# Kernel tuning notes

Hardware: AMD Instinct MI355X
Metric: run time of the kernel (lower is better)

The kernel has to match this reference:

```python
import jax, jax.numpy as jnp
import numpy as np

INPUT_SIZE = 512
HIDDEN = 1024
OUT = 4
SEQ = 2048


def setup_inputs() -> dict:
    key = jax.random.key(0)
    ks = jax.random.split(key, 12)
    s_in = 1.0 / np.sqrt(INPUT_SIZE)
    s_h = 1.0 / np.sqrt(HIDDEN)
    inp = {
        "x": jax.random.normal(ks[0], (SEQ, INPUT_SIZE), jnp.float32),
        "h0": jnp.zeros((1, 1, HIDDEN), jnp.float32),
        "c0": jnp.zeros((1, 1, HIDDEN), jnp.float32),
        # LSTM params (PyTorch layout: gates ordered i, f, g, o along 4H)
        "w_ih": jax.random.uniform(ks[1], (4 * HIDDEN, INPUT_SIZE), jnp.float32, -s_h, s_h),
        "w_hh": jax.random.uniform(ks[2], (4 * HIDDEN, HIDDEN), jnp.float32, -s_h, s_h),
        "b_ih": jax.random.uniform(ks[3], (4 * HIDDEN,), jnp.float32, -s_h, s_h),
        "b_hh": jax.random.uniform(ks[4], (4 * HIDDEN,), jnp.float32, -s_h, s_h),
        "fc1_w": jax.random.uniform(ks[5], (HIDDEN, HIDDEN), jnp.float32, -s_h, s_h),
        "fc1_b": jax.random.uniform(ks[6], (HIDDEN,), jnp.float32, -s_h, s_h),
        "fc2_w": jax.random.uniform(ks[7], (HIDDEN, HIDDEN), jnp.float32, -s_h, s_h),
        "fc2_b": jax.random.uniform(ks[8], (HIDDEN,), jnp.float32, -s_h, s_h),
        "mean_w": jax.random.uniform(ks[9], (OUT, HIDDEN), jnp.float32, -s_h, s_h),
        "mean_b": jax.random.uniform(ks[10], (OUT,), jnp.float32, -s_h, s_h),
        "log_std": jnp.zeros((OUT,), jnp.float32),
    }
    return inp


def _lstm(x, h0, c0, w_ih, w_hh, b_ih, b_hh):
    # Precompute input projections for all timesteps: [T, 4H]
    gx = x @ w_ih.T + b_ih + b_hh
    H = h0.shape[-1]

    def step(carry, gx_t):
        h, c = carry  # [H], [H]
        g = gx_t + h @ w_hh.T  # [4H]
        i = jax.nn.sigmoid(g[0 * H:1 * H])
        f = jax.nn.sigmoid(g[1 * H:2 * H])
        gg = jnp.tanh(g[2 * H:3 * H])
        o = jax.nn.sigmoid(g[3 * H:4 * H])
        c_new = f * c + i * gg
        h_new = o * jnp.tanh(c_new)
        return (h_new, c_new), h_new

    (hT, cT), ys = jax.lax.scan(step, (h0[0, 0], c0[0, 0]), gx)
    return ys, hT[None, None, :], cT[None, None, :]  # ys: [T, H]


def reference(x, h0, c0, w_ih, w_hh, b_ih, b_hh, fc1_w, fc1_b, fc2_w, fc2_b, mean_w, mean_b, log_std):
    ys, hT, cT = _lstm(x, h0, c0, w_ih, w_hh, b_ih, b_hh)
    h1 = jax.nn.relu(ys @ fc1_w.T + fc1_b)
    h2 = jax.nn.relu(h1 @ fc2_w.T + fc2_b)
    action_mean = h2 @ mean_w.T + mean_b  # [T, OUT]
    action_log_std = jnp.broadcast_to(log_std, action_mean.shape)
    return action_mean, action_log_std, hT, cT
```

## Files before the change

kernel.cpp:

```cpp
#include <hip/hip_runtime.h>
#include <stdint.h>


#define T_SEQ 2048
#define H 1024
#define G4 4096
#define K_IN 512
#define SENT 0x7FC0DEADu

__device__ __forceinline__ float sigmoidf_(float x) { return 1.0f / (1.0f + __expf(-x)); }
__device__ __forceinline__ float tanhf_(float x) { return 1.0f - 2.0f / (1.0f + __expf(2.0f * x)); }

__global__ void init_k(const float* __restrict__ h0, float* __restrict__ h_hist) {
  int idx = blockIdx.x * blockDim.x + threadIdx.x;
  if (idx < H) {
    h_hist[idx] = h0[idx];
  } else if (idx < (T_SEQ + 1) * H) {
    ((unsigned*)h_hist)[idx] = SENT;
  }
}

#define BM 64
#define BN 64
#define BK 32
#define LDT 68

template <bool RELU, bool HASB2>
__global__ __launch_bounds__(256) void gemm_bias_k(
    const float* __restrict__ A, const float* __restrict__ Bw,
    const float* __restrict__ b1, const float* __restrict__ b2,
    float* __restrict__ C, int M, int N, int K) {
  __shared__ float As[BK][LDT];
  __shared__ float Bs[BK][LDT];
  const int tid = threadIdx.x;
  const int m0 = blockIdx.y * BM;
  const int n0 = blockIdx.x * BN;
  const int tx = tid & 15, ty = tid >> 4;
  const int srow = tid >> 2;
  const int skq = tid & 3;

  float acc[4][4];
#pragma unroll
  for (int i = 0; i < 4; i++)
#pragma unroll
    for (int j = 0; j < 4; j++) acc[i][j] = 0.f;

  const float* Arow = A + (size_t)(m0 + srow) * K;
  const float* Brow = Bw + (size_t)(n0 + srow) * K;

  for (int k0 = 0; k0 < K; k0 += BK) {
    float4 a0 = *(const float4*)(Arow + k0 + skq * 8);
    float4 a1 = *(const float4*)(Arow + k0 + skq * 8 + 4);
    float4 c0_ = *(const float4*)(Brow + k0 + skq * 8);
    float4 c1_ = *(const float4*)(Brow + k0 + skq * 8 + 4);
    __syncthreads();
    const int kb = skq * 8;
    As[kb + 0][srow] = a0.x; As[kb + 1][srow] = a0.y; As[kb + 2][srow] = a0.z; As[kb + 3][srow] = a0.w;
    As[kb + 4][srow] = a1.x; As[kb + 5][srow] = a1.y; As[kb + 6][srow] = a1.z; As[kb + 7][srow] = a1.w;
    Bs[kb + 0][srow] = c0_.x; Bs[kb + 1][srow] = c0_.y; Bs[kb + 2][srow] = c0_.z; Bs[kb + 3][srow] = c0_.w;
    Bs[kb + 4][srow] = c1_.x; Bs[kb + 5][srow] = c1_.y; Bs[kb + 6][srow] = c1_.z; Bs[kb + 7][srow] = c1_.w;
    __syncthreads();
#pragma unroll
    for (int kk = 0; kk < BK; kk++) {
      float av[4], bv[4];
      *(float4*)av = *(const float4*)&As[kk][ty * 4];
      *(float4*)bv = *(const float4*)&Bs[kk][tx * 4];
#pragma unroll
      for (int i = 0; i < 4; i++)
#pragma unroll
        for (int j = 0; j < 4; j++) acc[i][j] = fmaf(av[i], bv[j], acc[i][j]);
    }
  }

  float bb[4];
#pragma unroll
  for (int j = 0; j < 4; j++) {
    bb[j] = b1[n0 + tx * 4 + j];
    if (HASB2) bb[j] += b2[n0 + tx * 4 + j];
  }
#pragma unroll
  for (int i = 0; i < 4; i++) {
    float4 o;
    float* op = (float*)&o;
#pragma unroll
    for (int j = 0; j < 4; j++) {
      float v = acc[i][j] + bb[j];
      op[j] = RELU ? fmaxf(v, 0.f) : v;
    }
    *(float4*)&C[(size_t)(m0 + ty * 4 + i) * N + n0 + tx * 4] = o;
  }
}

#define NWG 128
#define NTHR 512

__global__ __launch_bounds__(NTHR, 2) void lstm_k(
    const float* __restrict__ gx, const float* __restrict__ w_hh,
    const float* __restrict__ c0, float* __restrict__ h_hist,
    float* __restrict__ out) {
  unsigned* h_u = (unsigned*)h_hist;
  __shared__ float hbuf[H];
  __shared__ float partial[8][32];
  const int tid = threadIdx.x;
  const int wg = blockIdx.x;
  const int wave = tid >> 6, lane = tid & 63;
  const int row = lane & 31;
  const int seg = wave * 2 + (lane >> 5);
  const int g = row >> 3, u = row & 7;
  const int grow = g * 1024 + wg * 8 + u;

  float4 wreg[16];
  {
    const float* wp = w_hh + (size_t)grow * H + seg * 64;
#pragma unroll
    for (int j = 0; j < 16; j++) wreg[j] = *(const float4*)(wp + j * 4);
  }
  float c = 0.f;
  if (wave == 0 && lane < 8) c = c0[wg * 8 + lane];

  const int i0 = tid * 2;
  for (int t = 0; t < T_SEQ; t++) {
    float gxv = 0.f;
    if (wave == 0) gxv = gx[(size_t)t * G4 + grow];

    {
      unsigned* src = h_u + (size_t)t * H;
      unsigned a, b;
      do {
        a = __hip_atomic_load(&src[i0], __ATOMIC_RELAXED, __HIP_MEMORY_SCOPE_AGENT);
      } while (a == SENT);
      do {
        b = __hip_atomic_load(&src[i0 + 1], __ATOMIC_RELAXED, __HIP_MEMORY_SCOPE_AGENT);
      } while (b == SENT);
      hbuf[i0] = __uint_as_float(a);
      hbuf[i0 + 1] = __uint_as_float(b);
    }
    __syncthreads();

    float accv = 0.f;
    const float* hs = &hbuf[seg * 64];
#pragma unroll
    for (int j = 0; j < 16; j++) {
      float4 hv = *(const float4*)(hs + j * 4);
      float4 w = wreg[j];
      accv = fmaf(w.x, hv.x, accv);
      accv = fmaf(w.y, hv.y, accv);
      accv = fmaf(w.z, hv.z, accv);
      accv = fmaf(w.w, hv.w, accv);
    }
    accv += __shfl_down(accv, 32);
    if (lane < 32) partial[wave][lane] = accv;
    __syncthreads();

    if (wave == 0) {
      const int wsel = lane >> 5;
      float s = partial[wsel * 4 + 0][row] + partial[wsel * 4 + 1][row] +
                partial[wsel * 4 + 2][row] + partial[wsel * 4 + 3][row];
      s += __shfl_down(s, 32);
      float pre = s + gxv;
      float act = (g == 2) ? tanhf_(pre) : sigmoidf_(pre);
      float iv = __shfl(act, u);
      float fv = __shfl(act, 8 + u);
      float gv = __shfl(act, 16 + u);
      float ov = __shfl(act, 24 + u);
      if (lane < 8) {
        c = fmaf(fv, c, iv * gv);
        float hn = ov * tanhf_(c);
        __hip_atomic_store(&h_u[(size_t)(t + 1) * H + wg * 8 + lane],
                           __float_as_uint(hn), __ATOMIC_RELAXED,
                           __HIP_MEMORY_SCOPE_AGENT);
        if (t == T_SEQ - 1) {
          out[16384 + wg * 8 + lane] = hn;
          out[17408 + wg * 8 + lane] = c;
        }
      }
    }
  }
}

__global__ __launch_bounds__(256) void head_k(
    const float* __restrict__ h2, const float* __restrict__ mean_w,
    const float* __restrict__ mean_b, const float* __restrict__ log_std,
    float* __restrict__ out) {
  const int t = blockIdx.x;
  const int tid = threadIdx.x;
  const int wave = tid >> 6, lane = tid & 63;
  const float* hr = h2 + (size_t)t * H;
  const float* wr = mean_w + (size_t)wave * H;
  float s = 0.f;
#pragma unroll
  for (int j = 0; j < 16; j++) s = fmaf(hr[lane + j * 64], wr[lane + j * 64], s);
#pragma unroll
  for (int off = 32; off > 0; off >>= 1) s += __shfl_down(s, off);
  if (lane == 0) out[t * 4 + wave] = s + mean_b[wave];
  if (tid < 4) out[8192 + t * 4 + tid] = log_std[tid];
}

extern "C" void kernel_launch(void* const* d_in, const int* in_sizes, int n_in,
                              void* d_out, int out_size, void* d_ws, size_t ws_size,
                              hipStream_t stream) {
  const float* x      = (const float*)d_in[0];
  const float* h0     = (const float*)d_in[1];
  const float* c0     = (const float*)d_in[2];
  const float* w_ih   = (const float*)d_in[3];
  const float* w_hh   = (const float*)d_in[4];
  const float* b_ih   = (const float*)d_in[5];
  const float* b_hh   = (const float*)d_in[6];
  const float* fc1_w  = (const float*)d_in[7];
  const float* fc1_b  = (const float*)d_in[8];
  const float* fc2_w  = (const float*)d_in[9];
  const float* fc2_b  = (const float*)d_in[10];
  const float* mean_w = (const float*)d_in[11];
  const float* mean_b = (const float*)d_in[12];
  const float* lstd   = (const float*)d_in[13];
  float* out = (float*)d_out;

  float* gx = (float*)d_ws;
  float* h_hist = gx + (size_t)T_SEQ * G4;
  float* h1 = gx;
  float* h2 = gx + (size_t)T_SEQ * H;

  init_k<<<dim3((T_SEQ + 1) * H / 256), 256, 0, stream>>>(h0, h_hist);
  gemm_bias_k<false, true><<<dim3(G4 / BN, T_SEQ / BM), 256, 0, stream>>>(
      x, w_ih, b_ih, b_hh, gx, T_SEQ, G4, K_IN);
  lstm_k<<<dim3(NWG), NTHR, 0, stream>>>(gx, w_hh, c0, h_hist, out);
  gemm_bias_k<true, false><<<dim3(H / BN, T_SEQ / BM), 256, 0, stream>>>(
      h_hist + H, fc1_w, fc1_b, nullptr, h1, T_SEQ, H, H);
  gemm_bias_k<true, false><<<dim3(H / BN, T_SEQ / BM), 256, 0, stream>>>(
      h1, fc2_w, fc2_b, nullptr, h2, T_SEQ, H, H);
  head_k<<<dim3(T_SEQ), 256, 0, stream>>>(h2, mean_w, mean_b, lstd, out);
}
```

Measured before the change: 4.411 ms.

## Restructure LSTM recurrence to one hidden unit per wave with shuffle reductions

The persistent LSTM kernel is remapped so each wave owns one hidden unit, with lanes split across four gates and sixteen K segments, on 256 workgroups of 256 threads. The cross-wave partial-sum pass and its second __syncthreads per timestep are replaced by an intra-wave xor-shuffle reduction and in-register gate combination. It also polls h with 64-bit atomic loads, double-buffers padded LDS, and keeps 64 weights per lane in registers. The goal is a shorter critical path per timestep. In exchange it uses more workgroups polling global memory and more registers per lane.

```diff
diff --git a/kernel.cpp b/kernel.cpp
--- a/kernel.cpp
+++ b/kernel.cpp
@@ -91,88 +91,88 @@
   }
 }
 
-#define NWG 128
-#define NTHR 512
-
-__global__ __launch_bounds__(NTHR, 2) void lstm_k(
+#define NWG 256
+#define NTHR 256
+#define HPAD 68
+
+__global__ __launch_bounds__(NTHR) void lstm_k(
     const float* __restrict__ gx, const float* __restrict__ w_hh,
     const float* __restrict__ c0, float* __restrict__ h_hist,
     float* __restrict__ out) {
   unsigned* h_u = (unsigned*)h_hist;
-  __shared__ float hbuf[H];
-  __shared__ float partial[8][32];
+  __shared__ float hbuf[2][16 * HPAD];
   const int tid = threadIdx.x;
   const int wg = blockIdx.x;
   const int wave = tid >> 6, lane = tid & 63;
-  const int row = lane & 31;
-  const int seg = wave * 2 + (lane >> 5);
-  const int g = row >> 3, u = row & 7;
-  const int grow = g * 1024 + wg * 8 + u;
-
-  float4 wreg[16];
+  const int g = lane & 3;
+  const int s = lane >> 2;
+  const int unit = wg * 4 + wave;
+  const int grow = g * 1024 + unit;
+
+  float wreg[64];
   {
-    const float* wp = w_hh + (size_t)grow * H + seg * 64;
-#pragma unroll
-    for (int j = 0; j < 16; j++) wreg[j] = *(const float4*)(wp + j * 4);
-  }
-  float c = 0.f;
-  if (wave == 0 && lane < 8) c = c0[wg * 8 + lane];
-
-  const int i0 = tid * 2;
+    const float* wp = w_hh + (size_t)grow * H + s * 64;
+#pragma unroll
+    for (int j = 0; j < 64; j += 4) {
+      float4 w4 = *(const float4*)(wp + j);
+      wreg[j] = w4.x; wreg[j + 1] = w4.y; wreg[j + 2] = w4.z; wreg[j + 3] = w4.w;
+    }
+#pragma unroll
+    for (int j = 0; j < 64; j++) asm volatile("" : "+v"(wreg[j]));
+  }
+  float c = c0[unit];
+
+  const int stage_idx = 4 * tid + (tid >> 4) * 4;
   for (int t = 0; t < T_SEQ; t++) {
-    float gxv = 0.f;
-    if (wave == 0) gxv = gx[(size_t)t * G4 + grow];
+    const int buf = t & 1;
+    float gxv = gx[(size_t)t * G4 + grow];
+    asm volatile("" : "+v"(gxv));
 
     {
-      unsigned* src = h_u + (size_t)t * H;
-      unsigned a, b;
-      do {
-        a = __hip_atomic_load(&src[i0], __ATOMIC_RELAXED, __HIP_MEMORY_SCOPE_AGENT);
-      } while (a == SENT);
-      do {
-        b = __hip_atomic_load(&src[i0 + 1], __ATOMIC_RELAXED, __HIP_MEMORY_SCOPE_AGENT);
-      } while (b == SENT);
-      hbuf[i0] = __uint_as_float(a);
-      hbuf[i0 + 1] = __uint_as_float(b);
+      uint64_t* src = (uint64_t*)(h_u + (size_t)t * H) + tid * 2;
+      uint64_t a = __hip_atomic_load(&src[0], __ATOMIC_RELAXED, __HIP_MEMORY_SCOPE_AGENT);
+      uint64_t b = __hip_atomic_load(&src[1], __ATOMIC_RELAXED, __HIP_MEMORY_SCOPE_AGENT);
+      while ((unsigned)a == SENT || (unsigned)(a >> 32) == SENT)
+        a = __hip_atomic_load(&src[0], __ATOMIC_RELAXED, __HIP_MEMORY_SCOPE_AGENT);
+      while ((unsigned)b == SENT || (unsigned)(b >> 32) == SENT)
+        b = __hip_atomic_load(&src[1], __ATOMIC_RELAXED, __HIP_MEMORY_SCOPE_AGENT);
+      float4 v;
+      v.x = __uint_as_float((unsigned)a);
+      v.y = __uint_as_float((unsigned)(a >> 32));
+      v.z = __uint_as_float((unsigned)b);
+      v.w = __uint_as_float((unsigned)(b >> 32));
+      *(float4*)&hbuf[buf][stage_idx] = v;
     }
     __syncthreads();
 
-    float accv = 0.f;
-    const float* hs = &hbuf[seg * 64];
+    float acc0 = 0.f, acc1 = 0.f, acc2 = 0.f, acc3 = 0.f;
+    const float* hs = &hbuf[buf][s * HPAD];
 #pragma unroll
     for (int j = 0; j < 16; j++) {
       float4 hv = *(const float4*)(hs + j * 4);
-      float4 w = wreg[j];
-      accv = fmaf(w.x, hv.x, accv);
-      accv = fmaf(w.y, hv.y, accv);
-      accv = fmaf(w.z, hv.z, accv);
-      accv = fmaf(w.w, hv.w, accv);
-    }
-    accv += __shfl_down(accv, 32);
-    if (lane < 32) partial[wave][lane] = accv;
-    __syncthreads();
-
-    if (wave == 0) {
-      const int wsel = lane >> 5;
-      float s = partial[wsel * 4 + 0][row] + partial[wsel * 4 + 1][row] +
-                partial[wsel * 4 + 2][row] + partial[wsel * 4 + 3][row];
-      s += __shfl_down(s, 32);
-      float pre = s + gxv;
-      float act = (g == 2) ? tanhf_(pre) : sigmoidf_(pre);
-      float iv = __shfl(act, u);
-      float fv = __shfl(act, 8 + u);
-      float gv = __shfl(act, 16 + u);
-      float ov = __shfl(act, 24 + u);
-      if (lane < 8) {
-        c = fmaf(fv, c, iv * gv);
-        float hn = ov * tanhf_(c);
-        __hip_atomic_store(&h_u[(size_t)(t + 1) * H + wg * 8 + lane],
-                           __float_as_uint(hn), __ATOMIC_RELAXED,
-                           __HIP_MEMORY_SCOPE_AGENT);
-        if (t == T_SEQ - 1) {
-          out[16384 + wg * 8 + lane] = hn;
-          out[17408 + wg * 8 + lane] = c;
-        }
+      acc0 = fmaf(wreg[4 * j + 0], hv.x, acc0);
+      acc1 = fmaf(wreg[4 * j + 1], hv.y, acc1);
+      acc2 = fmaf(wreg[4 * j + 2], hv.z, acc2);
+      acc3 = fmaf(wreg[4 * j + 3], hv.w, acc3);
+    }
+    float accv = (acc0 + acc1) + (acc2 + acc3);
+    accv += __shfl_xor(accv, 4);
+    accv += __shfl_xor(accv, 8);
+    accv += __shfl_xor(accv, 16);
+    accv += __shfl_xor(accv, 32);
+    float pre = accv + gxv;
+    float act = (g == 2) ? tanhf_(pre) : sigmoidf_(pre);
+    float b1v = __shfl_xor(act, 1);
+    float b2v = __shfl_xor(act, 2);
+    float b3v = __shfl_xor(act, 3);
+    c = fmaf(b1v, c, act * b2v);
+    float hn = b3v * tanhf_(c);
+    if (lane == 0) {
+      __hip_atomic_store(&h_u[(size_t)(t + 1) * H + unit], __float_as_uint(hn),
+                         __ATOMIC_RELAXED, __HIP_MEMORY_SCOPE_AGENT);
+      if (t == T_SEQ - 1) {
+        out[16384 + unit] = hn;
+        out[17408 + unit] = c;
       }
     }
   }
```

After: 4.772 ms. 1.08x slower.
